# Optimization experiments

Hardware: AMD Instinct MI355X
Metric: run time of the kernel (lower is better)

The kernel has to match this reference:

```python
import jax, jax.numpy as jnp
import numpy as np

NUM_HEADS = 4
OUT_DIM = 64
IN_DIM = 128

def setup_inputs() -> dict:
    key = jax.random.key(0)
    k1, k2, k3, k4 = jax.random.split(key, 4)
    h = jax.random.normal(k1, (4, 256, IN_DIM), dtype=jnp.float32)
    adj = jax.random.randint(k2, (4, 256, 256), 0, 2).astype(jnp.int32)
    W = jax.random.normal(k3, (IN_DIM, NUM_HEADS * OUT_DIM), dtype=jnp.float32) * (1.0 / np.sqrt(IN_DIM))
    a = jax.random.normal(k4, (2 * OUT_DIM, 1), dtype=jnp.float32) * 0.1
    return {"h": h, "adj": adj, "W": W, "a": a}

def reference(h, adj, W, a):
    B, N, _ = h.shape
    H, D = NUM_HEADS, OUT_DIM
    Wh = (h @ W).reshape(B, N, H, D)                      # [B,N,H,D]
    # Exact replication of the torch repeat/view construction (row-major, same as torch.view)
    a1 = jnp.tile(Wh, (1, 1, 1, N)).reshape(B, N * H, N, D)
    a2 = jnp.tile(Wh, (1, N, 1, 1)).reshape(B, N * H, N, D)
    a_input = jnp.concatenate([a1, a2], axis=3)           # [B,N*H,N,2D]
    e = jax.nn.leaky_relu((a_input @ a)[..., 0], negative_slope=0.2)
    e = e.reshape(B, H, N, N)
    mask = adj[:, None, :, :] == 0                        # broadcast over heads
    attention = jax.nn.softmax(jnp.where(mask, -jnp.inf, e), axis=3)  # [B,H,N,N]
    h_prime = jnp.einsum('bhij,bjhd->bihd', attention, Wh)             # [B,N,H,D]
    return h_prime.reshape(B, N, H * D)
```

## Files before the change

kernel.cpp:

```cpp
#include <hip/hip_runtime.h>


typedef __attribute__((ext_vector_type(8))) short bf16x8;
typedef __attribute__((ext_vector_type(4))) float f32x4;

__device__ __forceinline__ short bf1(float x) {
  unsigned u = __builtin_bit_cast(unsigned, x);
  u = (u + 0x7FFFu + ((u >> 16) & 1u)) >> 16;
  return (short)u;
}
__device__ __forceinline__ bf16x8 pack8(float4 a, float4 b) {
  bf16x8 r;
  r[0]=bf1(a.x); r[1]=bf1(a.y); r[2]=bf1(a.z); r[3]=bf1(a.w);
  r[4]=bf1(b.x); r[5]=bf1(b.y); r[6]=bf1(b.z); r[7]=bf1(b.w);
  return r;
}

__global__ __launch_bounds__(256) void gat_prep(
    const float* __restrict__ h, const float* __restrict__ W,
    const float* __restrict__ a,
    short* __restrict__ WhT, float* __restrict__ f1g, float* __restrict__ f2g)
{
  const int tid  = threadIdx.x;
  const int lane = tid & 63;
  const int quad = lane >> 4, col = lane & 15;
  const int wv   = tid >> 6;
  const int blk  = blockIdx.x;
  const int ms = blk & 15, nt = (blk >> 4) & 3, b = blk >> 6;

  __shared__ short WbT[64][136];
  __shared__ float f1p[16][4];
  __shared__ float f2p[16][4];

  float4 wl[8];
#pragma unroll
  for (int q = 0; q < 8; q++) {
    const int idx = q * 256 + tid;
    const int k = idx >> 4, c4 = idx & 15;
    wl[q] = *(const float4*)(W + k * 256 + nt * 64 + c4 * 4);
  }
  const float* hrow = h + (b*256 + ms*16 + col) * 128 + quad*8;
  float4 hv[8];
#pragma unroll
  for (int kk = 0; kk < 4; kk++) {
    hv[2*kk]   = *(const float4*)(hrow + kk*32);
    hv[2*kk+1] = *(const float4*)(hrow + kk*32 + 4);
  }
  const float a1v = a[wv*16 + col];
  const float a2v = a[64 + wv*16 + col];

#pragma unroll
  for (int q = 0; q < 8; q++) {
    const int idx = q * 256 + tid;
    const int k = idx >> 4, c4 = idx & 15;
    WbT[c4*4 + 0][k] = bf1(wl[q].x);
    WbT[c4*4 + 1][k] = bf1(wl[q].y);
    WbT[c4*4 + 2][k] = bf1(wl[q].z);
    WbT[c4*4 + 3][k] = bf1(wl[q].w);
  }
  __syncthreads();

  f32x4 acc = {0.f, 0.f, 0.f, 0.f};
#pragma unroll
  for (int kk = 0; kk < 4; kk++) {
    bf16x8 bw = *(const bf16x8*)&WbT[wv*16 + col][kk*32 + quad*8];
    acc = __builtin_amdgcn_mfma_f32_16x16x32_bf16(pack8(hv[2*kk], hv[2*kk+1]), bw, acc, 0, 0, 0);
  }
  {
    const int dcol = nt*64 + wv*16 + col;
    const int n0   = ms*16 + quad*4;
    int2 pk;
    pk.x = (int)((unsigned)(unsigned short)bf1(acc[0]) |
                 ((unsigned)(unsigned short)bf1(acc[1]) << 16));
    pk.y = (int)((unsigned)(unsigned short)bf1(acc[2]) |
                 ((unsigned)(unsigned short)bf1(acc[3]) << 16));
    *(int2*)(WhT + b*65536 + dcol*256 + n0) = pk;
  }
#pragma unroll
  for (int r = 0; r < 4; r++) {
    float v1 = acc[r] * a1v;
    float v2 = acc[r] * a2v;
#pragma unroll
    for (int off = 1; off < 16; off <<= 1) {
      v1 += __shfl_xor(v1, off, 64);
      v2 += __shfl_xor(v2, off, 64);
    }
    if (col == 0) {
      const int row = quad*4 + r;
      f1p[row][wv] = v1;
      f2p[row][wv] = v2;
    }
  }
  __syncthreads();

  if (tid < 16) {
    const float s = f1p[tid][0] + f1p[tid][1] + f1p[tid][2] + f1p[tid][3];
    f1g[b*1024 + (ms*16 + tid)*4 + nt] = s;
  } else if (tid >= 64 && tid < 80) {
    const int n = tid - 64;
    const float s = f2p[n][0] + f2p[n][1] + f2p[n][2] + f2p[n][3];
    f2g[b*1024 + (ms*16 + n)*4 + nt] = s;
  }
}

__global__ __launch_bounds__(256) void gat_attn(
    const short* __restrict__ WhT, const float* __restrict__ f1g,
    const float* __restrict__ f2g, const int* __restrict__ adj,
    float* __restrict__ out)
{
  const int tid  = threadIdx.x;
  const int lane = tid & 63;
  const int quad = lane >> 4, col = lane & 15;
  const int wv   = tid >> 6;
  const int blk  = blockIdx.x;
  const int it = blk & 15, hp = (blk >> 4) & 3, b = blk >> 6;
  const int i0 = it * 16;

  __shared__ short attb[16][264];

  bf16x8 bv[8];
  const short* bp = WhT + b*65536 + (hp*64 + wv*16 + col)*256 + quad*8;
#pragma unroll
  for (int kk = 0; kk < 8; kk++) bv[kk] = *(const bf16x8*)(bp + kk*32);

  float4 f2v[4]; int4 av[4]; float f1s[4];
#pragma unroll
  for (int rq = 0; rq < 4; rq++) {
    const int i = i0 + wv*4 + rq;
    f2v[rq] = *(const float4*)(f2g + b*1024 + rq*256 + lane*4);
    av[rq]  = *(const int4*)(adj + (b*256 + i)*256 + lane*4);
    f1s[rq] = f1g[b*1024 + hp*256 + i];
  }

#pragma unroll
  for (int rq = 0; rq < 4; rq++) {
    const int rr = wv*4 + rq;
    const float s1v = f1s[rq];
    float e0 = s1v + f2v[rq].x, e1 = s1v + f2v[rq].y;
    float e2 = s1v + f2v[rq].z, e3 = s1v + f2v[rq].w;
    e0 = e0 > 0.f ? e0 : 0.2f*e0;  e1 = e1 > 0.f ? e1 : 0.2f*e1;
    e2 = e2 > 0.f ? e2 : 0.2f*e2;  e3 = e3 > 0.f ? e3 : 0.2f*e3;
    e0 = av[rq].x ? e0 : -1e30f;  e1 = av[rq].y ? e1 : -1e30f;
    e2 = av[rq].z ? e2 : -1e30f;  e3 = av[rq].w ? e3 : -1e30f;
    float x0 = __expf(e0), x1 = __expf(e1);
    float x2 = __expf(e2), x3 = __expf(e3);
    int2 pk2;
    pk2.x = (int)((unsigned)(unsigned short)bf1(x0) |
                  ((unsigned)(unsigned short)bf1(x1) << 16));
    pk2.y = (int)((unsigned)(unsigned short)bf1(x2) |
                  ((unsigned)(unsigned short)bf1(x3) << 16));
    *(int2*)&attb[rr][lane*4] = pk2;
  }
  __syncthreads();

  bf16x8 af[8];
#pragma unroll
  for (int kk = 0; kk < 8; kk++)
    af[kk] = *(const bf16x8*)&attb[col][kk*32 + quad*8];

  bf16x8 ones;
#pragma unroll
  for (int j = 0; j < 8; j++) ones[j] = (short)0x3F80;

  f32x4 acc0 = {0.f,0.f,0.f,0.f}, acc1 = {0.f,0.f,0.f,0.f};
  f32x4 sum0 = {0.f,0.f,0.f,0.f}, sum1 = {0.f,0.f,0.f,0.f};
#pragma unroll
  for (int kk = 0; kk < 4; kk++) {
    acc0 = __builtin_amdgcn_mfma_f32_16x16x32_bf16(af[kk],   bv[kk],   acc0, 0, 0, 0);
    acc1 = __builtin_amdgcn_mfma_f32_16x16x32_bf16(af[kk+4], bv[kk+4], acc1, 0, 0, 0);
    sum0 = __builtin_amdgcn_mfma_f32_16x16x32_bf16(af[kk],   ones,     sum0, 0, 0, 0);
    sum1 = __builtin_amdgcn_mfma_f32_16x16x32_bf16(af[kk+4], ones,     sum1, 0, 0, 0);
  }
#pragma unroll
  for (int r = 0; r < 4; r++) {
    const int m = quad*4 + r;
    out[(b*256 + i0 + m)*256 + hp*64 + wv*16 + col] =
        (acc0[r] + acc1[r]) / (sum0[r] + sum1[r]);
  }
}

extern "C" void kernel_launch(void* const* d_in, const int* in_sizes, int n_in,
                              void* d_out, int out_size, void* d_ws, size_t ws_size,
                              hipStream_t stream) {
  const float* h   = (const float*)d_in[0];
  const int*   adj = (const int*)d_in[1];
  const float* W   = (const float*)d_in[2];
  const float* a   = (const float*)d_in[3];
  float* out = (float*)d_out;

  short* WhT = (short*)d_ws;
  float* f1g = (float*)((char*)d_ws + 4*256*256*2);
  float* f2g = f1g + 4*1024;

  gat_prep<<<256, 256, 0, stream>>>(h, W, a, WhT, f1g, f2g);
  gat_attn<<<256, 256, 0, stream>>>(WhT, f1g, f2g, adj, out);
}
```

Before: 64.08 us.

## Fold attention vector into W and prefetch adjacency into L2 during prep

Each block in the prep kernel now computes W·a1 and W·a2 for its 64-column slice and stages them as bf16 in shared memory. Wave 0 then gets f1/f2 with one extra MFMA chain instead of shuffle reductions, a second shared-memory reduction and a second barrier. The prep kernel also loads the whole adjacency matrix (one int4 per thread) and pins it with an empty asm statement, so the attention kernel's adj reads are meant to hit cache. The cost is extra global reads of W and adj in the prep kernel, plus a small loss of precision from rounding W·a to bf16.

```diff
diff --git a/kernel.cpp b/kernel.cpp
--- a/kernel.cpp
+++ b/kernel.cpp
@@ -18,7 +18,7 @@
 
 __global__ __launch_bounds__(256) void gat_prep(
     const float* __restrict__ h, const float* __restrict__ W,
-    const float* __restrict__ a,
+    const float* __restrict__ a, const int* __restrict__ adj,
     short* __restrict__ WhT, float* __restrict__ f1g, float* __restrict__ f2g)
 {
   const int tid  = threadIdx.x;
@@ -29,8 +29,9 @@
   const int ms = blk & 15, nt = (blk >> 4) & 3, b = blk >> 6;
 
   __shared__ short WbT[64][136];
-  __shared__ float f1p[16][4];
-  __shared__ float f2p[16][4];
+  __shared__ short WaT16[16][136];
+
+  const int4 aw = ((const int4*)adj)[blk * 256 + tid];
 
   float4 wl[8];
 #pragma unroll
@@ -46,8 +47,21 @@
     hv[2*kk]   = *(const float4*)(hrow + kk*32);
     hv[2*kk+1] = *(const float4*)(hrow + kk*32 + 4);
   }
-  const float a1v = a[wv*16 + col];
-  const float a2v = a[64 + wv*16 + col];
+
+  {
+    const int k = tid >> 1, s = tid & 1;
+    const float4* wr = (const float4*)(W + k * 256 + nt * 64);
+    const float4* av = (const float4*)(a + s * 64);
+    float sacc = 0.f;
+#pragma unroll
+    for (int d4 = 0; d4 < 16; d4++) {
+      float4 x = wr[d4]; float4 y = av[d4];
+      sacc += x.x*y.x + x.y*y.y + x.z*y.z + x.w*y.w;
+    }
+    WaT16[s][k] = bf1(sacc);
+    int* zp = (int*)&WaT16[2][0];
+    for (int t = tid; t < 952; t += 256) zp[t] = 0;
+  }
 
 #pragma unroll
   for (int q = 0; q < 8; q++) {
@@ -60,11 +74,15 @@
   }
   __syncthreads();
 
+  bf16x8 afr[4];
+#pragma unroll
+  for (int kk = 0; kk < 4; kk++) afr[kk] = pack8(hv[2*kk], hv[2*kk+1]);
+
   f32x4 acc = {0.f, 0.f, 0.f, 0.f};
 #pragma unroll
   for (int kk = 0; kk < 4; kk++) {
     bf16x8 bw = *(const bf16x8*)&WbT[wv*16 + col][kk*32 + quad*8];
-    acc = __builtin_amdgcn_mfma_f32_16x16x32_bf16(pack8(hv[2*kk], hv[2*kk+1]), bw, acc, 0, 0, 0);
+    acc = __builtin_amdgcn_mfma_f32_16x16x32_bf16(afr[kk], bw, acc, 0, 0, 0);
   }
   {
     const int dcol = nt*64 + wv*16 + col;
@@ -76,31 +94,23 @@
                  ((unsigned)(unsigned short)bf1(acc[3]) << 16));
     *(int2*)(WhT + b*65536 + dcol*256 + n0) = pk;
   }
-#pragma unroll
-  for (int r = 0; r < 4; r++) {
-    float v1 = acc[r] * a1v;
-    float v2 = acc[r] * a2v;
-#pragma unroll
-    for (int off = 1; off < 16; off <<= 1) {
-      v1 += __shfl_xor(v1, off, 64);
-      v2 += __shfl_xor(v2, off, 64);
+
+  if (wv == 0) {
+    f32x4 accF = {0.f, 0.f, 0.f, 0.f};
+#pragma unroll
+    for (int kk = 0; kk < 4; kk++) {
+      bf16x8 bw = *(const bf16x8*)&WaT16[col][kk*32 + quad*8];
+      accF = __builtin_amdgcn_mfma_f32_16x16x32_bf16(afr[kk], bw, accF, 0, 0, 0);
     }
-    if (col == 0) {
-      const int row = quad*4 + r;
-      f1p[row][wv] = v1;
-      f2p[row][wv] = v2;
+    if (col < 2) {
+      float* dst = (col == 0) ? f1g : f2g;
+#pragma unroll
+      for (int r = 0; r < 4; r++)
+        dst[b*1024 + (ms*16 + quad*4 + r)*4 + nt] = accF[r];
     }
   }
-  __syncthreads();
-
-  if (tid < 16) {
-    const float s = f1p[tid][0] + f1p[tid][1] + f1p[tid][2] + f1p[tid][3];
-    f1g[b*1024 + (ms*16 + tid)*4 + nt] = s;
-  } else if (tid >= 64 && tid < 80) {
-    const int n = tid - 64;
-    const float s = f2p[n][0] + f2p[n][1] + f2p[n][2] + f2p[n][3];
-    f2g[b*1024 + (ms*16 + n)*4 + nt] = s;
-  }
+
+  asm volatile("" :: "v"(aw.x), "v"(aw.y), "v"(aw.z), "v"(aw.w));
 }
 
 __global__ __launch_bounds__(256) void gat_attn(
@@ -192,6 +202,6 @@
   float* f1g = (float*)((char*)d_ws + 4*256*256*2);
   float* f2g = f1g + 4*1024;
 
-  gat_prep<<<256, 256, 0, stream>>>(h, W, a, WhT, f1g, f2g);
+  gat_prep<<<256, 256, 0, stream>>>(h, W, a, adj, WhT, f1g, f2g);
   gat_attn<<<256, 256, 0, stream>>>(WhT, f1g, f2g, adj, out);
 }
```

New measurement: 65.23 us. No clear change (+1.8%).
